# Kernel tuning notes

Measured on AMD Instinct MI355X. Metric: run time of the kernel, lower is better.

Reference implementation:

```python
import jax, jax.numpy as jnp
import numpy as np

N_NODES = 50000
N_EDGES = 800000
D_IN = 8
D_MODEL = 128
N_CLASSES = 2


def gcn_conv(x, W, b, src, dst, n_nodes):
    # PyG GCNConv: h = x @ W; add self-loops; D^{-1/2} A D^{-1/2} aggregation; + bias
    h = x @ W  # [N, D]
    deg = jax.ops.segment_sum(jnp.ones(src.shape[0], h.dtype), dst, num_segments=n_nodes) + 1.0  # +1 self-loop
    dinv = jax.lax.rsqrt(deg)  # deg >= 1 always
    norm = dinv[src] * dinv[dst]  # [E]
    agg = jax.ops.segment_sum(h[src] * norm[:, None], dst, num_segments=n_nodes)
    agg = agg + h * (dinv * dinv)[:, None]  # self-loop term, norm_ii = dinv_i^2
    return agg + b


def setup_inputs() -> dict:
    key = jax.random.key(0)
    ks = jax.random.split(key, 10)
    x = jax.random.normal(ks[0], (N_NODES, D_IN), jnp.float32)
    edge_index = jax.random.randint(ks[1], (2, N_EDGES), 0, N_NODES, jnp.int64 if jax.config.jax_enable_x64 else jnp.int32)
    def glorot(k, shape):
        lim = np.sqrt(6.0 / (shape[0] + shape[1]))
        return jax.random.uniform(k, shape, jnp.float32, -lim, lim)
    return {
        "x": x,
        "edge_index": edge_index,
        "W1": glorot(ks[2], (D_IN, D_MODEL)),
        "b1": jnp.zeros((D_MODEL,), jnp.float32),
        "W2": glorot(ks[3], (D_MODEL, D_MODEL)),
        "b2": jnp.zeros((D_MODEL,), jnp.float32),
        "Wlin1": glorot(ks[4], (2 * D_MODEL, D_MODEL)),
        "blin1": jnp.zeros((D_MODEL,), jnp.float32),
        "Wfin": glorot(ks[5], (D_MODEL, N_CLASSES)),
        "bfin": jnp.zeros((N_CLASSES,), jnp.float32),
    }


def reference(x, edge_index, W1, b1, W2, b2, Wlin1, blin1, Wfin, bfin):
    src, dst = edge_index[0], edge_index[1]
    n = x.shape[0]
    h = jax.nn.relu(gcn_conv(x, W1, b1, src, dst, n))
    h = jax.nn.relu(gcn_conv(h, W2, b2, src, dst, n))
    xpair = jnp.concatenate((h[src], h[dst]), axis=1)  # [E, 2*D]
    xpair = jax.nn.relu(xpair @ Wlin1 + blin1)
    logits = xpair @ Wfin + bfin  # [E, C]
    return jax.nn.log_softmax(logits, axis=1)
```

## Files before the change

kernel.cpp:

```cpp
#include <hip/hip_runtime.h>
#include <stdint.h>
#include <math.h>

#define D 128

typedef unsigned short u16;
typedef __attribute__((ext_vector_type(8))) short bf16x8;
typedef __attribute__((ext_vector_type(4))) float f32x4;
typedef __attribute__((ext_vector_type(2))) float f32x2;

union BU { uint4 u; bf16x8 s; };

__device__ __forceinline__ unsigned f2bf_pk(float a, float b) {
    union { float f; unsigned u; } x, y; x.f = a; y.f = b;
    unsigned ra = x.u + 0x7FFF + ((x.u >> 16) & 1);
    unsigned rb = y.u + 0x7FFF + ((y.u >> 16) & 1);
    return (ra >> 16) | (rb & 0xFFFF0000u);
}
__device__ __forceinline__ u16 f2bf(float f) {
    union { float f; unsigned u; } x; x.f = f;
    unsigned r = x.u + 0x7FFF + ((x.u >> 16) & 1);
    return (u16)(r >> 16);
}
__device__ __forceinline__ f32x2 bf2f2v(unsigned u) {
    union { unsigned w[2]; f32x2 v; } t;
    t.w[0] = u << 16; t.w[1] = u & 0xFFFF0000u;
    return t.v;
}
__device__ __forceinline__ f32x2 vmax0(f32x2 a) {
    return __builtin_elementwise_max(a, (f32x2)(0.f));
}
__device__ __forceinline__ int padded4(int deg) {
    return (deg + 3) & ~3;
}


__global__ __launch_bounds__(256) void k_degree8(const int* __restrict__ dst, int E,
                                                 int* __restrict__ hist8, int* __restrict__ rank, int N) {
    int i = blockIdx.x * 256 + threadIdx.x;
    int copy = blockIdx.x & 7;
    int E4 = E >> 2;
    if (i < E4) {
        int4 d = ((const int4*)dst)[i];
        int* h = hist8 + copy * N;
        int4 rk;
        rk.x = atomicAdd(&h[d.x], 1);
        rk.y = atomicAdd(&h[d.y], 1);
        rk.z = atomicAdd(&h[d.z], 1);
        rk.w = atomicAdd(&h[d.w], 1);
        ((int4*)rank)[i] = rk;
    }
    if (i == 0) {
        for (int j = E4 * 4; j < E; ++j) rank[j] = atomicAdd(&hist8[dst[j]], 1);
    }
}

__global__ __launch_bounds__(256) void k_xcdoff_bsum(int* __restrict__ hist8, int* __restrict__ degi,
                                                     float* __restrict__ dinv, int* __restrict__ bsum, int N,
                                                     const float* __restrict__ x, float* __restrict__ xs) {
    __shared__ int ws[4];
    int t = threadIdx.x;
    int i = blockIdx.x * 256 + t;
    int pd = 0;
    if (i < N) {
        int run = 0;
#pragma unroll
        for (int j = 0; j < 8; ++j) {
            int c = hist8[j * N + i];
            hist8[j * N + i] = run;
            run += c;
        }
        degi[i] = run;
        float dv = rsqrtf((float)run + 1.0f);
        dinv[i] = dv;
        const float4* xp = (const float4*)(x + (size_t)i * 8);
        float4 a0 = xp[0], a1 = xp[1];
        float4 w0 = make_float4(dv * a0.x, dv * a0.y, dv * a0.z, dv * a0.w);
        float4 w1 = make_float4(dv * a1.x, dv * a1.y, dv * a1.z, dv * a1.w);
        float4* xo = (float4*)(xs + (size_t)i * 8);
        xo[0] = w0; xo[1] = w1;
        pd = padded4(run);
    } else if (i == N) {
        float4 z = make_float4(0.f, 0.f, 0.f, 0.f);
        float4* xo = (float4*)(xs + (size_t)N * 8);
        xo[0] = z; xo[1] = z;
    }
    int v = pd;
#pragma unroll
    for (int off = 1; off < 64; off <<= 1) v += __shfl_xor(v, off, 64);
    if ((t & 63) == 0) ws[t >> 6] = v;
    __syncthreads();
    if (t == 0) bsum[blockIdx.x] = ws[0] + ws[1] + ws[2] + ws[3];
}

__global__ __launch_bounds__(1024) void k_boff_wprep(const int* __restrict__ bsum, int* __restrict__ boff,
                                                     int nb, int* __restrict__ prow, int N,
                                                     const float* __restrict__ W2, const float* __restrict__ Wlin,
                                                     unsigned* __restrict__ wswz) {
    int t = threadIdx.x;
    if (blockIdx.x == 0) {
        __shared__ int s[1024];
        s[t] = (t < nb) ? bsum[t] : 0;
        __syncthreads();
        for (int off = 1; off < 1024; off <<= 1) {
            int v = (t >= off) ? s[t - off] : 0;
            __syncthreads();
            s[t] += v;
            __syncthreads();
        }
        if (t < nb) boff[t] = (t == 0) ? 0 : s[t - 1];
        if (t == 0) prow[N] = s[1023];
    } else {
        int tid = (blockIdx.x - 1) * 1024 + t;
        int m = tid >> 13;
        int r = tid & 8191;
        int jp = r & 3;
        int lane = (r >> 2) & 63;
        int ct = (r >> 8) & 7;
        int kc = r >> 11;
        int k0 = kc * 32 + (lane >> 4) * 8 + 2 * jp;
        int n = ct * 16 + (lane & 15);
        const float* srcp = (m == 0) ? W2 : (Wlin + (m - 1) * 16384);
        wswz[tid] = f2bf_pk(srcp[k0 * 128 + n], srcp[(k0 + 1) * 128 + n]);
    }
}

__global__ __launch_bounds__(256) void k_scan_final(const int* __restrict__ degi, const int* __restrict__ boff,
                                                    int* __restrict__ prow, int N, int* __restrict__ hist8) {
    __shared__ int s[256];
    int t = threadIdx.x;
    int i = blockIdx.x * 256 + t;
    int pd = (i < N) ? padded4(degi[i]) : 0;
    s[t] = pd;
    __syncthreads();
    for (int off = 1; off < 256; off <<= 1) {
        int v = (t >= off) ? s[t - off] : 0;
        __syncthreads();
        s[t] += v;
        __syncthreads();
    }
    if (i < N) {
        int p = boff[blockIdx.x] + ((t == 0) ? 0 : s[t - 1]);
        prow[i] = p;
#pragma unroll
        for (int j = 0; j < 8; ++j) hist8[j * N + i] += p;
    }
}


__global__ __launch_bounds__(256) void k_scatter_fill(
        const int* __restrict__ src, const int* __restrict__ dst, int E,
        const int* __restrict__ prow, const int* __restrict__ hist8, const int* __restrict__ rank,
        const int* __restrict__ degi,
        int* __restrict__ colsrc, int N, int eb4) {
    int t = threadIdx.x;
    int b = blockIdx.x;
    if (b < eb4) {
        int i = b * 256 + t;
        int E4 = E >> 2;
        if (i < E4) {
            int copy = b & 7;
            int4 d = ((const int4*)dst)[i];
            int4 s4 = ((const int4*)src)[i];
            int4 rk = ((const int4*)rank)[i];
            const int* h = hist8 + copy * N;
            colsrc[h[d.x] + rk.x] = s4.x;
            colsrc[h[d.y] + rk.y] = s4.y;
            colsrc[h[d.z] + rk.z] = s4.z;
            colsrc[h[d.w] + rk.w] = s4.w;
        }
        if (i == 0) {
            for (int j = E4 * 4; j < E; ++j)
                colsrc[hist8[dst[j]] + rank[j]] = src[j];
        }
    } else {
        int n = (b - eb4) * 256 + t;
        if (n < N) {
            int lo = prow[n];
            int deg = degi[n];
            int pd = padded4(deg);
            for (int j = deg; j < pd; ++j) colsrc[lo + j] = N;
        }
        if (b == eb4 && t == 0) {
            int P = prow[N];
            for (int j = 0; j < 16; ++j) colsrc[P + j] = N;
        }
    }
}

#define HROW 136


__global__ __launch_bounds__(256) void k_agg1gemm(
        const float* __restrict__ xs, const int* __restrict__ prow,
        const int* __restrict__ colsrc, const float* __restrict__ dinv,
        const float* __restrict__ b1, const float* __restrict__ W1,
        const uint4* __restrict__ wB0, u16* __restrict__ out0, int N) {
    __shared__ float W1s[8 * 128];
    __shared__ float b1s[128];
    __shared__ float ys[16][8];
    __shared__ u16 hs[16 * HROW];
    int t = threadIdx.x;
    int wv = t >> 6;
    int lane = t & 63;
    int sub = lane >> 4;
    int r = lane & 15;
    int base = blockIdx.x * 16;

    for (int idx = t; idx < 8 * 128; idx += 256) W1s[idx] = W1[idx];
    if (t < 128) b1s[t] = b1[t];

    int i = base + wv * 4 + sub;
    if (i < N) {
        float acc[8];
#pragma unroll
        for (int f = 0; f < 8; ++f) acc[f] = 0.f;
        int lo = prow[i], hiP = prow[i + 1];
        for (int k = lo + r; k < hiP; k += 16) {
            int cj = colsrc[k];
            const float4* xr = (const float4*)(xs + (size_t)cj * 8);
            float4 u0 = xr[0], u1 = xr[1];
            acc[0] += u0.x; acc[1] += u0.y; acc[2] += u0.z; acc[3] += u0.w;
            acc[4] += u1.x; acc[5] += u1.y; acc[6] += u1.z; acc[7] += u1.w;
        }
#pragma unroll
        for (int off = 1; off < 16; off <<= 1) {
#pragma unroll
            for (int f = 0; f < 8; ++f) acc[f] += __shfl_xor(acc[f], off, 64);
        }
        const float4* xi = (const float4*)(xs + (size_t)i * 8);
        float4 s0 = xi[0], s1 = xi[1];
        float di = dinv[i];
        acc[0] = di * (acc[0] + s0.x); acc[1] = di * (acc[1] + s0.y);
        acc[2] = di * (acc[2] + s0.z); acc[3] = di * (acc[3] + s0.w);
        acc[4] = di * (acc[4] + s1.x); acc[5] = di * (acc[5] + s1.y);
        acc[6] = di * (acc[6] + s1.z); acc[7] = di * (acc[7] + s1.w);
        if (r < 8) ys[wv * 4 + sub][r] = acc[r];
    }
    __syncthreads();

    {
        int node16 = t >> 4;
        int cseg = (t & 15) * 8;
        if (base + node16 < N) {
            float yv[8];
#pragma unroll
            for (int f = 0; f < 8; ++f) yv[f] = ys[node16][f];
            float o[8];
#pragma unroll
            for (int c = 0; c < 8; ++c) {
                float s = b1s[cseg + c];
#pragma unroll
                for (int f = 0; f < 8; ++f) s += yv[f] * W1s[f * 128 + cseg + c];
                o[c] = fmaxf(s, 0.f);
            }
            uint4 ov;
            ov.x = f2bf_pk(o[0], o[1]);
            ov.y = f2bf_pk(o[2], o[3]);
            ov.z = f2bf_pk(o[4], o[5]);
            ov.w = f2bf_pk(o[6], o[7]);
            *(uint4*)(hs + node16 * HROW + cseg) = ov;
        } else {
            *(uint4*)(hs + node16 * HROW + cseg) = make_uint4(0, 0, 0, 0);
        }
    }
    __syncthreads();

    int quad = lane >> 4;
    int l15 = lane & 15;
    int ct0 = wv * 2;

    f32x4 accA[2];
#pragma unroll
    for (int q = 0; q < 2; ++q) accA[q] = (f32x4){0.f, 0.f, 0.f, 0.f};

    const uint4* hrow = (const uint4*)(hs + l15 * HROW);
#pragma unroll
    for (int kc = 0; kc < 4; ++kc) {
        BU a; a.u = hrow[kc * 4 + quad];
#pragma unroll
        for (int q = 0; q < 2; ++q) {
            BU b0; b0.u = wB0[(kc * 8 + ct0 + q) * 64 + lane];
            accA[q] = __builtin_amdgcn_mfma_f32_16x16x32_bf16(a.s, b0.s, accA[q], 0, 0, 0);
        }
    }
#pragma unroll
    for (int reg = 0; reg < 4; ++reg) {
        int node = base + quad * 4 + reg;
        if (node >= N) continue;
        float sc = dinv[node];
#pragma unroll
        for (int q = 0; q < 2; ++q) {
            int colj = (ct0 + q) * 16 + l15;
            out0[(size_t)node * 128 + colj] = f2bf(accA[q][reg] * sc);
        }
    }
    if (blockIdx.x == 0 && t < 64) ((unsigned*)out0)[(size_t)N * 64 + t] = 0;
}


template <bool DUAL>
__global__ __launch_bounds__(256) void k_aggemm(const uint4* __restrict__ g, const int* __restrict__ prow,
                                                const int* __restrict__ colsrc, const float* __restrict__ dinv,
                                                const float* __restrict__ biasH,
                                                const uint4* __restrict__ wB0, const uint4* __restrict__ wB1,
                                                const float* __restrict__ bias1,
                                                u16* __restrict__ out0, u16* __restrict__ out1, int N) {
    __shared__ u16 hs[16 * HROW];
    int t = threadIdx.x;
    int wv = t >> 6;
    int lane = t & 63;
    int sub = lane >> 4;
    int r = lane & 15;
    int base = blockIdx.x * 16;

    for (int nd = 0; nd < 4; ++nd) {
        int i = base + wv * 4 + nd;
        int lrow = wv * 4 + nd;
        if (i < N) {
            f32x2 acc2[4];
#pragma unroll
            for (int j = 0; j < 4; ++j) acc2[j] = (f32x2)(0.f);
            int lo = prow[i], hiP = prow[i + 1];
            int idx = lo + sub;
            int c0 = colsrc[idx];
            int c1 = (idx + 4 < hiP) ? colsrc[idx + 4] : N;
            int c2 = (idx + 8 < hiP) ? colsrc[idx + 8] : N;
            uint4 v0 = g[c0 * 16 + r];
            uint4 v1 = g[c1 * 16 + r];
            for (int k = lo; k < hiP; k += 4) {
                int c3 = (idx + 12 < hiP) ? colsrc[idx + 12] : N;
                uint4 v2 = g[c2 * 16 + r];
                acc2[0] += bf2f2v(v0.x);
                acc2[1] += bf2f2v(v0.y);
                acc2[2] += bf2f2v(v0.z);
                acc2[3] += bf2f2v(v0.w);
                v0 = v1; v1 = v2; c2 = c3; idx += 4;
            }
#pragma unroll
            for (int j = 0; j < 4; ++j) {
                acc2[j].x += __shfl_xor(acc2[j].x, 16, 64);
                acc2[j].y += __shfl_xor(acc2[j].y, 16, 64);
                acc2[j].x += __shfl_xor(acc2[j].x, 32, 64);
                acc2[j].y += __shfl_xor(acc2[j].y, 32, 64);
            }
            if (sub == 0) {
                uint4 sv = g[i * 16 + r];
                acc2[0] += bf2f2v(sv.x);
                acc2[1] += bf2f2v(sv.y);
                acc2[2] += bf2f2v(sv.z);
                acc2[3] += bf2f2v(sv.w);
                float di = dinv[i];
                float4 b0 = ((const float4*)biasH)[r * 2];
                float4 b1v = ((const float4*)biasH)[r * 2 + 1];
                float r0 = fmaxf(acc2[0].x * di + b0.x, 0.f);
                float r1 = fmaxf(acc2[0].y * di + b0.y, 0.f);
                float r2 = fmaxf(acc2[1].x * di + b0.z, 0.f);
                float r3 = fmaxf(acc2[1].y * di + b0.w, 0.f);
                float r4 = fmaxf(acc2[2].x * di + b1v.x, 0.f);
                float r5 = fmaxf(acc2[2].y * di + b1v.y, 0.f);
                float r6 = fmaxf(acc2[3].x * di + b1v.z, 0.f);
                float r7 = fmaxf(acc2[3].y * di + b1v.w, 0.f);
                uint4 o;
                o.x = f2bf_pk(r0, r1);
                o.y = f2bf_pk(r2, r3);
                o.z = f2bf_pk(r4, r5);
                o.w = f2bf_pk(r6, r7);
                *(uint4*)(hs + lrow * HROW + r * 8) = o;
            }
        } else if (sub == 0) {
            *(uint4*)(hs + lrow * HROW + r * 8) = make_uint4(0, 0, 0, 0);
        }
    }
    __syncthreads();

    int quad = lane >> 4;
    int l15 = lane & 15;
    int ct0 = wv * 2;

    f32x4 accA[2], accB[2];
#pragma unroll
    for (int q = 0; q < 2; ++q) { accA[q] = (f32x4){0.f, 0.f, 0.f, 0.f}; accB[q] = (f32x4){0.f, 0.f, 0.f, 0.f}; }

    const uint4* hrow = (const uint4*)(hs + l15 * HROW);
#pragma unroll
    for (int kc = 0; kc < 4; ++kc) {
        BU a; a.u = hrow[kc * 4 + quad];
#pragma unroll
        for (int q = 0; q < 2; ++q) {
            BU b0; b0.u = wB0[(kc * 8 + ct0 + q) * 64 + lane];
            accA[q] = __builtin_amdgcn_mfma_f32_16x16x32_bf16(a.s, b0.s, accA[q], 0, 0, 0);
            if (DUAL) {
                BU b1; b1.u = wB1[(kc * 8 + ct0 + q) * 64 + lane];
                accB[q] = __builtin_amdgcn_mfma_f32_16x16x32_bf16(a.s, b1.s, accB[q], 0, 0, 0);
            }
        }
    }
#pragma unroll
    for (int reg = 0; reg < 4; ++reg) {
        int node = base + quad * 4 + reg;
        if (node >= N) continue;
        float sc = DUAL ? 1.0f : dinv[node];
#pragma unroll
        for (int q = 0; q < 2; ++q) {
            int colj = (ct0 + q) * 16 + l15;
            out0[(size_t)node * 128 + colj] = f2bf(accA[q][reg] * sc);
            if (DUAL) out1[(size_t)node * 128 + colj] = f2bf(accB[q][reg] + bias1[colj]);
        }
    }
    if (blockIdx.x == 0 && t < 64) ((unsigned*)out0)[(size_t)N * 64 + t] = 0;
}


__global__ __launch_bounds__(256) void k_edge(const uint4* __restrict__ a, const uint4* __restrict__ c,
                                              const int* __restrict__ src, const int* __restrict__ dst,
                                              const float* __restrict__ Wfin, const float* __restrict__ bfin,
                                              float* __restrict__ out, int E) {
    int t = threadIdx.x;
    int g = t >> 4;
    int r = t & 15;
    int base = blockIdx.x * 64 + g * 4;

    f32x2 wd[4];
    const float4* wvp = (const float4*)Wfin;
#pragma unroll
    for (int q = 0; q < 4; ++q) {
        float4 m = wvp[r * 4 + q];
        wd[q] = (f32x2){m.x - m.y, m.z - m.w};
    }
    float bd = bfin[0] - bfin[1];

    int4 s4, d4;
    if (base + 3 < E) {
        s4 = ((const int4*)src)[blockIdx.x * 16 + g];
        d4 = ((const int4*)dst)[blockIdx.x * 16 + g];
    } else {
        int e0 = base, e1 = base + 1, e2 = base + 2, e3 = base + 3;
        s4.x = (e0 < E) ? src[e0] : 0; d4.x = (e0 < E) ? dst[e0] : 0;
        s4.y = (e1 < E) ? src[e1] : 0; d4.y = (e1 < E) ? dst[e1] : 0;
        s4.z = (e2 < E) ? src[e2] : 0; d4.z = (e2 < E) ? dst[e2] : 0;
        s4.w = (e3 < E) ? src[e3] : 0; d4.w = (e3 < E) ? dst[e3] : 0;
    }

    uint4 av[4], cv[4];
    av[0] = a[(size_t)s4.x * 16 + r];  cv[0] = c[(size_t)d4.x * 16 + r];
    av[1] = a[(size_t)s4.y * 16 + r];  cv[1] = c[(size_t)d4.y * 16 + r];
    av[2] = a[(size_t)s4.z * 16 + r];  cv[2] = c[(size_t)d4.z * 16 + r];
    av[3] = a[(size_t)s4.w * 16 + r];  cv[3] = c[(size_t)d4.w * 16 + r];

    float dl[4];
#pragma unroll
    for (int j = 0; j < 4; ++j) {
        f32x2 p = (f32x2)(0.f);
        f32x2 z;
        z = vmax0(bf2f2v(av[j].x) + bf2f2v(cv[j].x)); p += z * wd[0];
        z = vmax0(bf2f2v(av[j].y) + bf2f2v(cv[j].y)); p += z * wd[1];
        z = vmax0(bf2f2v(av[j].z) + bf2f2v(cv[j].z)); p += z * wd[2];
        z = vmax0(bf2f2v(av[j].w) + bf2f2v(cv[j].w)); p += z * wd[3];
        dl[j] = p.x + p.y;
    }
#pragma unroll
    for (int off = 1; off < 16; off <<= 1) {
#pragma unroll
        for (int j = 0; j < 4; ++j) dl[j] += __shfl_xor(dl[j], off, 64);
    }
    if (r == 0) {
        float o[8];
#pragma unroll
        for (int j = 0; j < 4; ++j) {
            float dlt = dl[j] + bd;
            float tn = -fabsf(dlt);
            float s = __logf(1.f + __expf(tn));
            o[2 * j]     = (dlt >= 0.f) ? -s : (dlt - s);
            o[2 * j + 1] = (dlt >= 0.f) ? (-dlt - s) : -s;
        }
        if (base + 3 < E) {
            float4* op = (float4*)(out + 2 * (size_t)base);
            op[0] = make_float4(o[0], o[1], o[2], o[3]);
            op[1] = make_float4(o[4], o[5], o[6], o[7]);
        } else {
#pragma unroll
            for (int j = 0; j < 4; ++j) {
                if (base + j < E)
                    *((float2*)(out + 2 * (size_t)(base + j))) = make_float2(o[2 * j], o[2 * j + 1]);
            }
        }
    }
}

extern "C" void kernel_launch(void* const* d_in, const int* in_sizes, int n_in,
                              void* d_out, int out_size, void* d_ws, size_t ws_size,
                              hipStream_t stream) {
    const float* x     = (const float*)d_in[0];
    const int*   ei    = (const int*)d_in[1];
    const float* W1    = (const float*)d_in[2];
    const float* b1    = (const float*)d_in[3];
    const float* W2    = (const float*)d_in[4];
    const float* b2    = (const float*)d_in[5];
    const float* Wlin1 = (const float*)d_in[6];
    const float* blin1 = (const float*)d_in[7];
    const float* Wfin  = (const float*)d_in[8];
    const float* bfin  = (const float*)d_in[9];
    float* out = (float*)d_out;

    int N = in_sizes[0] / 8;
    int E = in_sizes[1] / 2;
    const int* src = ei;
    const int* dst = ei + E;
    int nb = (N + 255) / 256;
    int eb4 = (E / 4 + 255) / 256;

#define ALIGN256(p) (char*)(((uintptr_t)(p) + 255) & ~(uintptr_t)255)
    char* w = (char*)d_ws;
    int* hist8 = (int*)w;     w += (size_t)8 * N * 4;
    int* rank = (int*)w;      w += (size_t)E * 4;
    int* degi = (int*)w;      w += (size_t)N * 4;
    int* prow = (int*)w;      w += (size_t)(N + 1) * 4;
    float* dinv = (float*)w;  w += (size_t)N * 4;
    int* bsum = (int*)w;      w += (size_t)nb * 4;
    int* boff = (int*)w;      w += (size_t)nb * 4;
    w = ALIGN256(w);
    int* colsrc = (int*)w;    w += ((size_t)E + 8 * (size_t)N + 64) * 4;
    w = ALIGN256(w);
    unsigned* wswz = (unsigned*)w; w += (size_t)3 * 8192 * 4;
    w = ALIGN256(w);
    float* xs = (float*)w;    w += (size_t)(N + 1) * 8 * 4;
    w = ALIGN256(w);
    unsigned* bufA = (unsigned*)w; w += (size_t)(N + 1) * 64 * 4;
    w = ALIGN256(w);
    unsigned* bufC = (unsigned*)w; w += (size_t)N * 64 * 4;
    w = ALIGN256(w);
    unsigned* bufG2 = (unsigned*)w; w += (size_t)(N + 1) * 64 * 4;

    hipMemsetAsync(hist8, 0, (size_t)8 * N * 4, stream);

    k_degree8<<<eb4, 256, 0, stream>>>(dst, E, hist8, rank, N);
    k_xcdoff_bsum<<<nb, 256, 0, stream>>>(hist8, degi, dinv, bsum, N, x, xs);
    k_boff_wprep<<<25, 1024, 0, stream>>>(bsum, boff, nb, prow, N, W2, Wlin1, wswz);
    k_scan_final<<<nb, 256, 0, stream>>>(degi, boff, prow, N, hist8);
    k_scatter_fill<<<eb4 + nb, 256, 0, stream>>>(src, dst, E, prow, hist8, rank, degi,
                                                 colsrc, N, eb4);

    int ablocks = (N + 15) / 16;
    k_agg1gemm<<<ablocks, 256, 0, stream>>>(xs, prow, colsrc, dinv, b1, W1,
                                            (const uint4*)wswz, (u16*)bufG2, N);
    k_aggemm<true><<<ablocks, 256, 0, stream>>>((const uint4*)bufG2, prow, colsrc, dinv, b2,
                                                (const uint4*)(wswz + 8192), (const uint4*)(wswz + 16384),
                                                blin1, (u16*)bufA, (u16*)bufC, N);

    k_edge<<<(E + 63) / 64, 256, 0, stream>>>((const uint4*)bufA, (const uint4*)bufC,
                                              src, dst, Wfin, bfin, out, E);
}
```

Measured before the change: 253.2 us.

## Narrow CSR indices to 16-bit and fold weight prep and block scan into neighbouring kernels

Measured after the change: 246.8 us (median of 2 runs). 1.03x faster.

```diff
diff --git a/kernel.cpp b/kernel.cpp
--- a/kernel.cpp
+++ b/kernel.cpp
@@ -36,22 +36,41 @@
 
 
 __global__ __launch_bounds__(256) void k_degree8(const int* __restrict__ dst, int E,
-                                                 int* __restrict__ hist8, int* __restrict__ rank, int N) {
-    int i = blockIdx.x * 256 + threadIdx.x;
-    int copy = blockIdx.x & 7;
-    int E4 = E >> 2;
-    if (i < E4) {
-        int4 d = ((const int4*)dst)[i];
-        int* h = hist8 + copy * N;
-        int4 rk;
-        rk.x = atomicAdd(&h[d.x], 1);
-        rk.y = atomicAdd(&h[d.y], 1);
-        rk.z = atomicAdd(&h[d.z], 1);
-        rk.w = atomicAdd(&h[d.w], 1);
-        ((int4*)rank)[i] = rk;
-    }
-    if (i == 0) {
-        for (int j = E4 * 4; j < E; ++j) rank[j] = atomicAdd(&hist8[dst[j]], 1);
+                                                 int* __restrict__ hist8, u16* __restrict__ rank, int N,
+                                                 int eb4,
+                                                 const float* __restrict__ W2, const float* __restrict__ Wlin,
+                                                 unsigned* __restrict__ wswz) {
+    int b = blockIdx.x;
+    int t = threadIdx.x;
+    if (b < eb4) {
+        int i = b * 256 + t;
+        int copy = b & 7;
+        int E4 = E >> 2;
+        if (i < E4) {
+            int4 d = ((const int4*)dst)[i];
+            int* h = hist8 + copy * N;
+            ushort4 rk;
+            rk.x = (u16)atomicAdd(&h[d.x], 1);
+            rk.y = (u16)atomicAdd(&h[d.y], 1);
+            rk.z = (u16)atomicAdd(&h[d.z], 1);
+            rk.w = (u16)atomicAdd(&h[d.w], 1);
+            ((ushort4*)rank)[i] = rk;
+        }
+        if (i == 0) {
+            for (int j = E4 * 4; j < E; ++j) rank[j] = (u16)atomicAdd(&hist8[dst[j]], 1);
+        }
+    } else {
+        int tid = (b - eb4) * 256 + t;
+        int m = tid >> 13;
+        int r = tid & 8191;
+        int jp = r & 3;
+        int lane = (r >> 2) & 63;
+        int ct = (r >> 8) & 7;
+        int kc = r >> 11;
+        int k0 = kc * 32 + (lane >> 4) * 8 + 2 * jp;
+        int n = ct * 16 + (lane & 15);
+        const float* srcp = (m == 0) ? W2 : (Wlin + (m - 1) * 16384);
+        wswz[tid] = f2bf_pk(srcp[k0 * 128 + n], srcp[(k0 + 1) * 128 + n]);
     }
 }
 
@@ -93,42 +112,22 @@
     if (t == 0) bsum[blockIdx.x] = ws[0] + ws[1] + ws[2] + ws[3];
 }
 
-__global__ __launch_bounds__(1024) void k_boff_wprep(const int* __restrict__ bsum, int* __restrict__ boff,
-                                                     int nb, int* __restrict__ prow, int N,
-                                                     const float* __restrict__ W2, const float* __restrict__ Wlin,
-                                                     unsigned* __restrict__ wswz) {
-    int t = threadIdx.x;
-    if (blockIdx.x == 0) {
-        __shared__ int s[1024];
-        s[t] = (t < nb) ? bsum[t] : 0;
+__global__ __launch_bounds__(256) void k_scan_final(const int* __restrict__ degi, const int* __restrict__ bsum,
+                                                    int* __restrict__ prow, int N, int* __restrict__ hist8,
+                                                    int nb) {
+    __shared__ int s[256];
+    __shared__ int sb[256];
+    int t = threadIdx.x;
+    sb[t] = (t < nb) ? bsum[t] : 0;
+    __syncthreads();
+    for (int off = 1; off < 256; off <<= 1) {
+        int v = (t >= off) ? sb[t - off] : 0;
         __syncthreads();
-        for (int off = 1; off < 1024; off <<= 1) {
-            int v = (t >= off) ? s[t - off] : 0;
-            __syncthreads();
-            s[t] += v;
-            __syncthreads();
-        }
-        if (t < nb) boff[t] = (t == 0) ? 0 : s[t - 1];
-        if (t == 0) prow[N] = s[1023];
-    } else {
-        int tid = (blockIdx.x - 1) * 1024 + t;
-        int m = tid >> 13;
-        int r = tid & 8191;
-        int jp = r & 3;
-        int lane = (r >> 2) & 63;
-        int ct = (r >> 8) & 7;
-        int kc = r >> 11;
-        int k0 = kc * 32 + (lane >> 4) * 8 + 2 * jp;
-        int n = ct * 16 + (lane & 15);
-        const float* srcp = (m == 0) ? W2 : (Wlin + (m - 1) * 16384);
-        wswz[tid] = f2bf_pk(srcp[k0 * 128 + n], srcp[(k0 + 1) * 128 + n]);
-    }
-}
-
-__global__ __launch_bounds__(256) void k_scan_final(const int* __restrict__ degi, const int* __restrict__ boff,
-                                                    int* __restrict__ prow, int N, int* __restrict__ hist8) {
-    __shared__ int s[256];
-    int t = threadIdx.x;
+        sb[t] += v;
+        __syncthreads();
+    }
+    int boff = (blockIdx.x == 0) ? 0 : sb[blockIdx.x - 1];
+
     int i = blockIdx.x * 256 + t;
     int pd = (i < N) ? padded4(degi[i]) : 0;
     s[t] = pd;
@@ -140,19 +139,20 @@
         __syncthreads();
     }
     if (i < N) {
-        int p = boff[blockIdx.x] + ((t == 0) ? 0 : s[t - 1]);
+        int p = boff + ((t == 0) ? 0 : s[t - 1]);
         prow[i] = p;
 #pragma unroll
         for (int j = 0; j < 8; ++j) hist8[j * N + i] += p;
     }
+    if (blockIdx.x == (unsigned)(nb - 1) && t == 0) prow[N] = sb[nb - 1];
 }
 
 
 __global__ __launch_bounds__(256) void k_scatter_fill(
         const int* __restrict__ src, const int* __restrict__ dst, int E,
-        const int* __restrict__ prow, const int* __restrict__ hist8, const int* __restrict__ rank,
+        const int* __restrict__ prow, const int* __restrict__ hist8, const u16* __restrict__ rank,
         const int* __restrict__ degi,
-        int* __restrict__ colsrc, int N, int eb4) {
+        u16* __restrict__ colsrc, int N, int eb4) {
     int t = threadIdx.x;
     int b = blockIdx.x;
     if (b < eb4) {
@@ -162,16 +162,16 @@
             int copy = b & 7;
             int4 d = ((const int4*)dst)[i];
             int4 s4 = ((const int4*)src)[i];
-            int4 rk = ((const int4*)rank)[i];
+            ushort4 rk = ((const ushort4*)rank)[i];
             const int* h = hist8 + copy * N;
-            colsrc[h[d.x] + rk.x] = s4.x;
-            colsrc[h[d.y] + rk.y] = s4.y;
-            colsrc[h[d.z] + rk.z] = s4.z;
-            colsrc[h[d.w] + rk.w] = s4.w;
+            colsrc[h[d.x] + rk.x] = (u16)s4.x;
+            colsrc[h[d.y] + rk.y] = (u16)s4.y;
+            colsrc[h[d.z] + rk.z] = (u16)s4.z;
+            colsrc[h[d.w] + rk.w] = (u16)s4.w;
         }
         if (i == 0) {
             for (int j = E4 * 4; j < E; ++j)
-                colsrc[hist8[dst[j]] + rank[j]] = src[j];
+                colsrc[hist8[dst[j]] + rank[j]] = (u16)src[j];
         }
     } else {
         int n = (b - eb4) * 256 + t;
@@ -179,11 +179,11 @@
             int lo = prow[n];
             int deg = degi[n];
             int pd = padded4(deg);
-            for (int j = deg; j < pd; ++j) colsrc[lo + j] = N;
+            for (int j = deg; j < pd; ++j) colsrc[lo + j] = (u16)N;
         }
         if (b == eb4 && t == 0) {
             int P = prow[N];
-            for (int j = 0; j < 16; ++j) colsrc[P + j] = N;
+            for (int j = 0; j < 16; ++j) colsrc[P + j] = (u16)N;
         }
     }
 }
@@ -193,7 +193,7 @@
 
 __global__ __launch_bounds__(256) void k_agg1gemm(
         const float* __restrict__ xs, const int* __restrict__ prow,
-        const int* __restrict__ colsrc, const float* __restrict__ dinv,
+        const u16* __restrict__ colsrc, const float* __restrict__ dinv,
         const float* __restrict__ b1, const float* __restrict__ W1,
         const uint4* __restrict__ wB0, u16* __restrict__ out0, int N) {
     __shared__ float W1s[8 * 128];
@@ -301,7 +301,7 @@
 
 template <bool DUAL>
 __global__ __launch_bounds__(256) void k_aggemm(const uint4* __restrict__ g, const int* __restrict__ prow,
-                                                const int* __restrict__ colsrc, const float* __restrict__ dinv,
+                                                const u16* __restrict__ colsrc, const float* __restrict__ dinv,
                                                 const float* __restrict__ biasH,
                                                 const uint4* __restrict__ wB0, const uint4* __restrict__ wB1,
                                                 const float* __restrict__ bias1,
@@ -513,14 +513,14 @@
 #define ALIGN256(p) (char*)(((uintptr_t)(p) + 255) & ~(uintptr_t)255)
     char* w = (char*)d_ws;
     int* hist8 = (int*)w;     w += (size_t)8 * N * 4;
-    int* rank = (int*)w;      w += (size_t)E * 4;
+    u16* rank = (u16*)w;      w += (size_t)E * 2;
+    w = ALIGN256(w);
     int* degi = (int*)w;      w += (size_t)N * 4;
     int* prow = (int*)w;      w += (size_t)(N + 1) * 4;
     float* dinv = (float*)w;  w += (size_t)N * 4;
     int* bsum = (int*)w;      w += (size_t)nb * 4;
-    int* boff = (int*)w;      w += (size_t)nb * 4;
-    w = ALIGN256(w);
-    int* colsrc = (int*)w;    w += ((size_t)E + 8 * (size_t)N + 64) * 4;
+    w = ALIGN256(w);
+    u16* colsrc = (u16*)w;    w += ((size_t)E + 8 * (size_t)N + 64) * 2;
     w = ALIGN256(w);
     unsigned* wswz = (unsigned*)w; w += (size_t)3 * 8192 * 4;
     w = ALIGN256(w);
@@ -534,10 +534,9 @@
 
     hipMemsetAsync(hist8, 0, (size_t)8 * N * 4, stream);
 
-    k_degree8<<<eb4, 256, 0, stream>>>(dst, E, hist8, rank, N);
+    k_degree8<<<eb4 + 96, 256, 0, stream>>>(dst, E, hist8, rank, N, eb4, W2, Wlin1, wswz);
     k_xcdoff_bsum<<<nb, 256, 0, stream>>>(hist8, degi, dinv, bsum, N, x, xs);
-    k_boff_wprep<<<25, 1024, 0, stream>>>(bsum, boff, nb, prow, N, W2, Wlin1, wswz);
-    k_scan_final<<<nb, 256, 0, stream>>>(degi, boff, prow, N, hist8);
+    k_scan_final<<<nb, 256, 0, stream>>>(degi, bsum, prow, N, hist8, nb);
     k_scatter_fill<<<eb4 + nb, 256, 0, stream>>>(src, dst, E, prow, hist8, rank, degi,
                                                  colsrc, N, eb4);
 
```
